# Kernel tuning notes

Measured on AMD Instinct MI355X. Metric: run time of the kernel, lower is better.

Reference implementation:

```python
import jax, jax.numpy as jnp
import numpy as np

E = 512      # embedding_dim == head_dim
H = 8        # num_heads
F = E * H    # ffn_dim = 4096
B = 2
S = 2048
SCALE = float(np.sqrt(E))


def setup_inputs() -> dict:
    key = jax.random.key(0)
    kx, kq, kk, kv, ko = jax.random.split(key, 5)
    x = jax.random.normal(kx, (B, S, E), dtype=jnp.float32)
    # torch Linear weights: [out_features, in_features], y = x @ W.T
    w_std = 1.0 / np.sqrt(E)
    Wq = jax.random.normal(kq, (F, E), dtype=jnp.float32) * w_std
    Wk = jax.random.normal(kk, (F, E), dtype=jnp.float32) * w_std
    Wv = jax.random.normal(kv, (F, E), dtype=jnp.float32) * w_std
    Wo = jax.random.normal(ko, (E, F), dtype=jnp.float32) * (1.0 / np.sqrt(F))
    # causal mask: 1 where attended, 0 where masked (masked_fill(mask == 0, -inf))
    attn_mask = jnp.tril(jnp.ones((S, S), dtype=jnp.int32))[None, None]  # [1,1,S,S]
    return {"x": x, "attn_mask": attn_mask, "Wq": Wq, "Wk": Wk, "Wv": Wv, "Wo": Wo}


def reference(x, attn_mask, Wq, Wk, Wv, Wo):
    b, s, _ = x.shape
    # projections + split heads: [B,S,F] -> [B,S,H,E]
    q = (x @ Wq.T).reshape(b, s, H, E)
    k = (x @ Wk.T).reshape(b, s, H, E)
    v = (x @ Wv.T).reshape(b, s, H, E)
    # scaled dot-product scores [B,H,S,S]
    scores = jnp.einsum('bqhd,bkhd->bhqk', q, k) / SCALE
    scores = jnp.where(attn_mask == 0, -jnp.inf, scores)
    w = jax.nn.softmax(scores, axis=-1)
    # dropout rate 0.0 (eval) -> identity
    out = jnp.einsum('bhqk,bkhd->bqhd', w, v).reshape(b, s, F)
    return out @ Wo.T  # [B,S,E]
```

## Files before the change

kernel.cpp:

```cpp
#include <hip/hip_runtime.h>
#include <hip/hip_bf16.h>

typedef __attribute__((ext_vector_type(8))) short short8;
typedef __attribute__((ext_vector_type(4))) float f32x4;
typedef __attribute__((ext_vector_type(8))) unsigned short ushort8;

#define LDS_ASYNC16(gsrc, ldst) \
  __builtin_amdgcn_global_load_lds((const __attribute__((address_space(1))) void*)(gsrc), \
                                   (__attribute__((address_space(3))) void*)(ldst), 16, 0, 0)

__device__ __forceinline__ unsigned short f2bf(float f) {
  unsigned int u = __float_as_uint(f);
  unsigned int r = (u + 0x7FFFu + ((u >> 16) & 1u)) >> 16;
  return (unsigned short)r;
}
__device__ __forceinline__ float bf2f(unsigned short h) {
  return __uint_as_float((unsigned int)h << 16);
}

__global__ __launch_bounds__(256) void cast5_f32_bf16(
    const float* __restrict__ i0, const float* __restrict__ i1, const float* __restrict__ i2,
    const float* __restrict__ i3, const float* __restrict__ i4,
    unsigned short* __restrict__ out) {
  const float* src[5] = {i0, i1, i2, i3, i4};
  int z = blockIdx.z;
  const float* in = src[z];
  size_t i = ((size_t)blockIdx.x * 256 + threadIdx.x) * 8;
  float4 a = *(const float4*)(in + i);
  float4 b = *(const float4*)(in + i + 4);
  ushort8 o;
  o[0] = f2bf(a.x); o[1] = f2bf(a.y); o[2] = f2bf(a.z); o[3] = f2bf(a.w);
  o[4] = f2bf(b.x); o[5] = f2bf(b.y); o[6] = f2bf(b.z); o[7] = f2bf(b.w);
  *(ushort8*)(out + (size_t)z * 2097152 + i) = o;
}

__global__ __launch_bounds__(256) void transpose_v(const unsigned short* __restrict__ V,
                                                   unsigned short* __restrict__ Vt) {
  __shared__ unsigned short t[64][72];
  int slot = blockIdx.z;
  int k0 = blockIdx.x << 6, d0 = blockIdx.y << 6;
  const unsigned short* src = V + (size_t)k0 * 4096 + slot * 512 + d0;
  int rr = threadIdx.x >> 3;
  int cc = (threadIdx.x & 7) << 3;
#pragma unroll
  for (int half = 0; half < 64; half += 32) {
    int r = rr + half;
    ushort8 v = *(const ushort8*)(src + (size_t)r * 4096 + cc);
#pragma unroll
    for (int e = 0; e < 8; ++e) t[cc + e][r] = v[e];
  }
  __syncthreads();
  unsigned short* dst = Vt + ((size_t)slot * 512 + d0) * 2048 + k0;
#pragma unroll
  for (int half = 0; half < 64; half += 32) {
    int d = rr + half;
    *(ushort8*)(dst + (size_t)d * 2048 + cc) = *(const ushort8*)&t[d][cc];
  }
}

__global__ __launch_bounds__(256) void softmax_causal_bf16(unsigned short* __restrict__ S) {
  int row = blockIdx.x;
  int q = row & 2047;
  unsigned short* srow = S + (size_t)row * 2048;
  int n = q + 1;
  int nW = ((q >> 7) + 1) << 7;
  int t = threadIdx.x, wave = t >> 6, lane = t & 63;
  int base = t * 8;
  ushort8 u = {};
  if (base < nW) u = *(const ushort8*)(srow + base);
  float vals[8];
  float m = -1e30f;
#pragma unroll
  for (int e = 0; e < 8; ++e) {
    float v = bf2f(u[e]);
    vals[e] = (base + e < n) ? v : -1e30f;
    m = fmaxf(m, vals[e]);
  }
#pragma unroll
  for (int off = 32; off > 0; off >>= 1) m = fmaxf(m, __shfl_xor(m, off, 64));
  __shared__ float red[8];
  if (lane == 0) red[wave] = m;
  __syncthreads();
  m = fmaxf(fmaxf(red[0], red[1]), fmaxf(red[2], red[3]));
  float s = 0.f;
#pragma unroll
  for (int e = 0; e < 8; ++e) {
    float ex = (base + e < n) ? __expf(vals[e] - m) : 0.f;
    vals[e] = ex; s += ex;
  }
#pragma unroll
  for (int off = 32; off > 0; off >>= 1) s += __shfl_xor(s, off, 64);
  if (lane == 0) red[4 + wave] = s;
  __syncthreads();
  s = red[4] + red[5] + red[6] + red[7];
  float inv = 1.0f / s;
  if (base < nW) {
    ushort8 o;
#pragma unroll
    for (int e = 0; e < 8; ++e) o[e] = f2bf(vals[e] * inv);
    *(ushort8*)(srow + base) = o;
  }
}

__global__ __launch_bounds__(256) void reduce_k4(const float4* __restrict__ p,
                                                 float4* __restrict__ out, int n4) {
  int i = blockIdx.x * 256 + threadIdx.x;
  if (i >= n4) return;
  float4 a = p[i], b = p[i + n4], c = p[i + 2 * n4], d = p[i + 3 * n4];
  float4 o;
  o.x = (a.x + b.x) + (c.x + d.x);
  o.y = (a.y + b.y) + (c.y + d.y);
  o.z = (a.z + b.z) + (c.z + d.z);
  o.w = (a.w + b.w) + (c.w + d.w);
  out[i] = o;
}

#define STGU(u_)                                                                   \
  do {                                                                             \
    int kb_ = (u_) * 32;                                                           \
    unsigned short* Ad_ = AsBase + ((u_) & 3) * 8192 + tid * 8;                    \
    unsigned short* Bd_ = BsBase + ((u_) & 3) * 8192 + tid * 8;                    \
    LDS_ASYNC16(Ap + (size_t)(m0 + r0) * lda + kb_ + cs0, Ad_);                    \
    LDS_ASYNC16(Bp + (size_t)(n0 + r0) * ldb + kb_ + cs0, Bd_);                    \
    LDS_ASYNC16(Ap + (size_t)(m0 + r0 + 128) * lda + kb_ + cs0, Ad_ + 4096);       \
    LDS_ASYNC16(Bp + (size_t)(n0 + r0 + 128) * ldb + kb_ + cs0, Bd_ + 4096);       \
  } while (0)

#define UNITPH(u_, STAGE_, WAITOP_)                                                \
  {                                                                                \
    const unsigned short* Au = AsBase + ((u_) & 3) * 8192;                         \
    const unsigned short* Bu = BsBase + ((u_) & 3) * 8192;                         \
    short8 af[8], bf[4];                                                           \
    _Pragma("unroll") for (int j = 0; j < 8; ++j)                                  \
      af[j] = *(const short8*)(Au + (wm * 128 + j * 16 + lr) * 32 + sA);           \
    _Pragma("unroll") for (int j = 0; j < 4; ++j)                                  \
      bf[j] = *(const short8*)(Bu + (wn * 64 + j * 16 + lr) * 32 + sA);            \
    if (STAGE_) STGU((u_) + 3);                                                    \
    __builtin_amdgcn_s_barrier();                                                  \
    __builtin_amdgcn_s_setprio(1);                                                 \
    _Pragma("unroll") for (int j = 0; j < 8; ++j)                                  \
      _Pragma("unroll") for (int j2 = 0; j2 < 4; ++j2)                             \
        acc[j][j2] = __builtin_amdgcn_mfma_f32_16x16x32_bf16(af[j], bf[j2],        \
                                                             acc[j][j2], 0, 0, 0); \
    __builtin_amdgcn_s_setprio(0);                                                 \
    WAITOP_;                                                                       \
    __builtin_amdgcn_s_barrier();                                                  \
  }

template<int OUT_F32, int CSKIP>
__global__ __launch_bounds__(512, 2) void gemm8p(
    const unsigned short* __restrict__ A, const unsigned short* __restrict__ B,
    void* __restrict__ C, int K, int lda, int ldb, int ldc, int nH,
    long long sAb, long long sAh, long long sBb, long long sBh,
    long long sCb, long long sCh, float scale)
{
  __shared__ unsigned short AsBase[4 * 8192];
  __shared__ unsigned short BsBase[4 * 8192];
  int m0 = blockIdx.y * 256, n0 = blockIdx.x * 256;
  if (CSKIP && n0 > m0) return;
  int z = blockIdx.z;
  int zb = z / nH, zh = z - zb * nH;
  const unsigned short* Ap = A + (size_t)(zb * sAb + zh * sAh);
  const unsigned short* Bp = B + (size_t)(zb * sBb + zh * sBh);
  size_t coff = (size_t)(zb * sCb + zh * sCh);
  int tid = threadIdx.x;
  int wid = tid >> 6, lane = tid & 63;
  int wm = wid >> 2, wn = wid & 3;
  int lr = lane & 15, hi = lane >> 4;
  int sA  = (hi ^ ((lr >> 1) & 3)) << 3;
  int r0  = tid >> 2;
  int cs0 = ((tid & 3) ^ ((r0 >> 1) & 3)) << 3;

  int N = K >> 5;
  f32x4 acc[8][4] = {};

  STGU(0); STGU(1); STGU(2);
  asm volatile("s_waitcnt vmcnt(8)" ::: "memory");
  __builtin_amdgcn_s_barrier();

  for (int u = 0; u + 3 < N; ++u)
    UNITPH(u, 1, asm volatile("s_waitcnt vmcnt(8)" ::: "memory"))
  UNITPH(N - 3, 0, asm volatile("s_waitcnt vmcnt(4)" ::: "memory"))
  UNITPH(N - 2, 0, asm volatile("s_waitcnt vmcnt(0)" ::: "memory"))
  UNITPH(N - 1, 0, )

#pragma unroll
  for (int m = 0; m < 8; ++m)
#pragma unroll
    for (int n = 0; n < 4; ++n)
#pragma unroll
      for (int r = 0; r < 4; ++r) {
        int row = m0 + wm * 128 + m * 16 + hi * 4 + r;
        int col = n0 + wn * 64 + n * 16 + lr;
        float v = acc[m][n][r] * scale;
        if (OUT_F32) ((float*)C)[coff + (size_t)row * ldc + col] = v;
        else ((unsigned short*)C)[coff + (size_t)row * ldc + col] = f2bf(v);
      }
}

template<int OUT_F32, int CSKIP, int KCLIP>
__global__ __launch_bounds__(256, 2) void gemm_bt(
    const unsigned short* __restrict__ A, const unsigned short* __restrict__ B,
    void* __restrict__ C, int K, int lda, int ldb, int ldc, int nH,
    long long sAb, long long sAh, long long sBb, long long sBh,
    long long sCb, long long sCh, float scale)
{
  __shared__ unsigned short As[128 * 64];
  __shared__ unsigned short Bs[128 * 64];
  int m0 = blockIdx.y * 128, n0 = blockIdx.x * 128;
  if (CSKIP && n0 > m0) return;
  int z = blockIdx.z;
  int zb = z / nH, zh = z - zb * nH;
  const unsigned short* Ap = A + (size_t)(zb * sAb + zh * sAh);
  const unsigned short* Bp = B + (size_t)(zb * sBb + zh * sBh);
  size_t coff = (size_t)(zb * sCb + zh * sCh);
  int tid = threadIdx.x;
  int wave = tid >> 6, lane = tid & 63;
  int kEnd = KCLIP ? min(K, m0 + 128) : K;

  int wr = (wave >> 1) * 64, wc = (wave & 1) * 64;
  int lr = lane & 15;
  int lkb = (lane >> 4) * 8;

  f32x4 acc[4][4] = {};

  for (int k0 = 0; k0 < kEnd; k0 += 64) {
#pragma unroll
    for (int it = 0; it < 4; ++it) {
      int g = it * 256 + tid;
      int r = g >> 3, c = (g & 7) << 3;
      LDS_ASYNC16(Ap + (size_t)(m0 + r) * lda + (k0 + c), As + (size_t)(it * 256 + wave * 64) * 8);
      LDS_ASYNC16(Bp + (size_t)(n0 + r) * ldb + (k0 + c), Bs + (size_t)(it * 256 + wave * 64) * 8);
    }
    __syncthreads();
#pragma unroll
    for (int kk = 0; kk < 64; kk += 32) {
      short8 a[4], b[4];
#pragma unroll
      for (int i = 0; i < 4; ++i)
        a[i] = *(const short8*)(As + (size_t)(wr + i * 16 + lr) * 64 + kk + lkb);
#pragma unroll
      for (int j = 0; j < 4; ++j)
        b[j] = *(const short8*)(Bs + (size_t)(wc + j * 16 + lr) * 64 + kk + lkb);
#pragma unroll
      for (int i = 0; i < 4; ++i)
#pragma unroll
        for (int j = 0; j < 4; ++j)
          acc[i][j] = __builtin_amdgcn_mfma_f32_16x16x32_bf16(a[i], b[j], acc[i][j], 0, 0, 0);
    }
    __syncthreads();
  }

  int orow = (lane >> 4) * 4, ocol = lane & 15;
#pragma unroll
  for (int i = 0; i < 4; ++i)
#pragma unroll
    for (int j = 0; j < 4; ++j)
#pragma unroll
      for (int r = 0; r < 4; ++r) {
        int row = m0 + wr + i * 16 + orow + r;
        int col = n0 + wc + j * 16 + ocol;
        float v = acc[i][j][r] * scale;
        if (OUT_F32) ((float*)C)[coff + (size_t)row * ldc + col] = v;
        else ((unsigned short*)C)[coff + (size_t)row * ldc + col] = f2bf(v);
      }
}

extern "C" void kernel_launch(void* const* d_in, const int* in_sizes, int n_in,
                              void* d_out, int out_size, void* d_ws, size_t ws_size,
                              hipStream_t stream) {
  const float* x  = (const float*)d_in[0];
  const float* Wq = (const float*)d_in[2];
  const float* Wk = (const float*)d_in[3];
  const float* Wv = (const float*)d_in[4];
  const float* Wo = (const float*)d_in[5];

  if (ws_size < (size_t)188 * (1 << 20)) return;

  char* ws = (char*)d_ws;
  unsigned short* xb   = (unsigned short*)(ws);
  unsigned short* Wob  = (unsigned short*)(ws + (size_t)16  * (1 << 20));
  unsigned short* QKV  = (unsigned short*)(ws + (size_t)20  * (1 << 20));
  unsigned short* Sc   = (unsigned short*)(ws + (size_t)116 * (1 << 20));
  unsigned short* Vt   = (unsigned short*)(ws);
  float*          Pp   = (float*)(ws + (size_t)116 * (1 << 20));

  const int NEw = 4096 * 512;
  const long long NEm = 4096LL * 4096;

  cast5_f32_bf16<<<dim3(1024, 1, 5), 256, 0, stream>>>(x, Wq, Wk, Wv, Wo, xb);

  gemm8p<0, 0><<<dim3(16, 16, 3), 512, 0, stream>>>(
      xb, xb + NEw, QKV, 512, 512, 512, 4096, 3,
      0LL, 0LL, 0LL, (long long)NEw, 0LL, NEm, 1.0f);

  for (int b = 0; b < 2; ++b) {
    size_t tokOff = (size_t)b * 2048 * 4096;
    const unsigned short* Qb = QKV + tokOff;
    const unsigned short* Kb = QKV + NEm + tokOff;
    const unsigned short* Vb = QKV + 2 * NEm + tokOff;
    unsigned short* AOb = QKV + tokOff;

    gemm8p<0, 1><<<dim3(8, 8, 8), 512, 0, stream>>>(
        Qb, Kb, Sc, 512, 4096, 4096, 2048, 8,
        0LL, 512LL, 0LL, 512LL, 0LL, 2048LL * 2048, 0.04419417382415922f);

    transpose_v<<<dim3(32, 8, 8), 256, 0, stream>>>(Vb, Vt);

    softmax_causal_bf16<<<dim3(8 * 2048), 256, 0, stream>>>(Sc);

    gemm_bt<0, 0, 1><<<dim3(4, 16, 8), 256, 0, stream>>>(
        Sc, Vt, AOb, 2048, 2048, 2048, 4096, 8,
        0LL, 2048LL * 2048, 0LL, 512LL * 2048, 0LL, 512LL, 1.0f);
  }

  gemm_bt<1, 0, 0><<<dim3(4, 32, 4), 256, 0, stream>>>(
      QKV, Wob, Pp, 1024, 4096, 4096, 512, 4,
      0LL, 1024LL, 0LL, 1024LL, 0LL, 2097152LL, 1.0f);

  reduce_k4<<<dim3(2048), 256, 0, stream>>>((const float4*)Pp, (float4*)d_out, 524288);
}
```

Measured before the change: 346.4 us.

## Double-buffer MFMA fragments in gemm8p and hardcode a 16-step K loop

The gemm8p main loop now reads LDS fragments for the next K-step into a second register set while MFMAs run on the current set. This cuts the barriers per step from two to one and hides LDS read latency behind matrix math. The loop is fully unrolled for a fixed 16 steps (K=512), and the K argument is no longer used. This raises register pressure, and any launch with a different K would give wrong results.

```diff
diff --git a/kernel.cpp b/kernel.cpp
--- a/kernel.cpp
+++ b/kernel.cpp
@@ -126,31 +126,33 @@
     LDS_ASYNC16(Bp + (size_t)(n0 + r0 + 128) * ldb + kb_ + cs0, Bd_ + 4096);       \
   } while (0)
 
-#define UNITPH(u_, STAGE_, WAITOP_)                                                \
+#define RDFR(u_, AF, BF)                                                           \
   {                                                                                \
-    const unsigned short* Au = AsBase + ((u_) & 3) * 8192;                         \
-    const unsigned short* Bu = BsBase + ((u_) & 3) * 8192;                         \
-    short8 af[8], bf[4];                                                           \
-    _Pragma("unroll") for (int j = 0; j < 8; ++j)                                  \
-      af[j] = *(const short8*)(Au + (wm * 128 + j * 16 + lr) * 32 + sA);           \
-    _Pragma("unroll") for (int j = 0; j < 4; ++j)                                  \
-      bf[j] = *(const short8*)(Bu + (wn * 64 + j * 16 + lr) * 32 + sA);            \
-    if (STAGE_) STGU((u_) + 3);                                                    \
-    __builtin_amdgcn_s_barrier();                                                  \
-    __builtin_amdgcn_s_setprio(1);                                                 \
-    _Pragma("unroll") for (int j = 0; j < 8; ++j)                                  \
-      _Pragma("unroll") for (int j2 = 0; j2 < 4; ++j2)                             \
-        acc[j][j2] = __builtin_amdgcn_mfma_f32_16x16x32_bf16(af[j], bf[j2],        \
-                                                             acc[j][j2], 0, 0, 0); \
-    __builtin_amdgcn_s_setprio(0);                                                 \
-    WAITOP_;                                                                       \
-    __builtin_amdgcn_s_barrier();                                                  \
-  }
+    const unsigned short* Au_ = AsBase + ((u_) & 3) * 8192;                        \
+    const unsigned short* Bu_ = BsBase + ((u_) & 3) * 8192;                        \
+    _Pragma("unroll") for (int j_ = 0; j_ < 8; ++j_)                               \
+      AF[j_] = *(const short8*)(Au_ + (wm * 128 + j_ * 16 + lr) * 32 + sA);        \
+    _Pragma("unroll") for (int j_ = 0; j_ < 4; ++j_)                               \
+      BF[j_] = *(const short8*)(Bu_ + (wn * 64 + j_ * 16 + lr) * 32 + sA);         \
+  }
+
+#define MMAC(AF, BF)                                                               \
+  __builtin_amdgcn_s_setprio(1);                                                   \
+  _Pragma("unroll") for (int j_ = 0; j_ < 8; ++j_)                                 \
+    _Pragma("unroll") for (int j2_ = 0; j2_ < 4; ++j2_)                            \
+      acc[j_][j2_] = __builtin_amdgcn_mfma_f32_16x16x32_bf16(AF[j_], BF[j2_],      \
+                                                             acc[j_][j2_], 0, 0, 0); \
+  __builtin_amdgcn_s_setprio(0);
+
+#define VMC4() asm volatile("s_waitcnt vmcnt(4)" ::: "memory")
+#define VMC0() asm volatile("s_waitcnt vmcnt(0)" ::: "memory")
+#define VMC8() asm volatile("s_waitcnt vmcnt(8)" ::: "memory")
+#define BARR() __builtin_amdgcn_s_barrier()
 
 template<int OUT_F32, int CSKIP>
 __global__ __launch_bounds__(512, 2) void gemm8p(
     const unsigned short* __restrict__ A, const unsigned short* __restrict__ B,
-    void* __restrict__ C, int K, int lda, int ldb, int ldc, int nH,
+    void* __restrict__ C, int K , int lda, int ldb, int ldc, int nH,
     long long sAb, long long sAh, long long sBb, long long sBh,
     long long sCb, long long sCh, float scale)
 {
@@ -171,18 +173,22 @@
   int r0  = tid >> 2;
   int cs0 = ((tid & 3) ^ ((r0 >> 1) & 3)) << 3;
 
-  int N = K >> 5;
+  short8 af0[8], bf0[4], af1[8], bf1[4];
   f32x4 acc[8][4] = {};
 
   STGU(0); STGU(1); STGU(2);
-  asm volatile("s_waitcnt vmcnt(8)" ::: "memory");
-  __builtin_amdgcn_s_barrier();
-
-  for (int u = 0; u + 3 < N; ++u)
-    UNITPH(u, 1, asm volatile("s_waitcnt vmcnt(8)" ::: "memory"))
-  UNITPH(N - 3, 0, asm volatile("s_waitcnt vmcnt(4)" ::: "memory"))
-  UNITPH(N - 2, 0, asm volatile("s_waitcnt vmcnt(0)" ::: "memory"))
-  UNITPH(N - 1, 0, )
+  VMC8(); BARR();
+  RDFR(0, af0, bf0);
+  VMC4(); BARR();
+
+  for (int u = 0; u < 12; u += 2) {
+    RDFR(u + 1, af1, bf1); STGU(u + 3); MMAC(af0, bf0); VMC4(); BARR();
+    RDFR(u + 2, af0, bf0); STGU(u + 4); MMAC(af1, bf1); VMC4(); BARR();
+  }
+  RDFR(13, af1, bf1); STGU(15); MMAC(af0, bf0); VMC4(); BARR();
+  RDFR(14, af0, bf0);           MMAC(af1, bf1); VMC0(); BARR();
+  RDFR(15, af1, bf1);           MMAC(af0, bf0);         BARR();
+                                MMAC(af1, bf1);
 
 #pragma unroll
   for (int m = 0; m < 8; ++m)
```

Result: no change. 339.9 us (median of 2 runs) (-1.9%).
